# Performance work log

Hardware: AMD Instinct MI355X
Metric: run time of the kernel (lower is better)

## Reference

```python
import jax, jax.numpy as jnp
import numpy as np

EMBED_DIM = 768
N_HEADS = 12
HEAD_DIM = EMBED_DIM // N_HEADS


def setup_inputs() -> dict:
    key = jax.random.key(0)
    ks = jax.random.split(key, 5)
    s = 1.0 / np.sqrt(EMBED_DIM)
    x = jax.random.normal(ks[0], (8, 1024, EMBED_DIM), dtype=jnp.float32)
    w_qkv = jax.random.normal(ks[1], (EMBED_DIM, 3 * EMBED_DIM), dtype=jnp.float32) * s
    b_qkv = jnp.zeros((3 * EMBED_DIM,), dtype=jnp.float32)
    w_proj = jax.random.normal(ks[2], (EMBED_DIM, EMBED_DIM), dtype=jnp.float32) * s
    b_proj = jnp.zeros((EMBED_DIM,), dtype=jnp.float32)
    return {"x": x, "w_qkv": w_qkv, "b_qkv": b_qkv, "w_proj": w_proj, "b_proj": b_proj}


def reference(x, w_qkv, b_qkv, w_proj, b_proj):
    B, S, D = x.shape
    H, Hd = N_HEADS, HEAD_DIM
    qkv = x @ w_qkv + b_qkv                      # [B,S,3D]
    qkv = qkv.reshape(B, S, 3, H, Hd).transpose(2, 0, 3, 1, 4)  # [3,B,H,S,Hd]
    q, k, v = qkv[0], qkv[1], qkv[2]
    scale = Hd ** -0.5
    attn = jnp.einsum('bhqd,bhkd->bhqk', q, k) * scale  # [B,H,S,S]
    attn = jax.nn.softmax(attn, axis=-1)
    out = jnp.einsum('bhqk,bhkd->bhqd', attn, v)        # [B,H,S,Hd]
    out = out.transpose(0, 2, 1, 3).reshape(B, S, D)
    return out @ w_proj + b_proj
```

## Files before the change

kernel.cpp:

```cpp
#include <hip/hip_runtime.h>
#include <stdint.h>

typedef unsigned short ushort_t;
typedef __bf16 bf16x8 __attribute__((ext_vector_type(8)));
typedef float floatx4 __attribute__((ext_vector_type(4)));

#define B_   8
#define S_   1024
#define D_   768
#define H_   12
#define M_   (B_ * S_)
#define N3_  (3 * D_)
#define QK_  1536

static __device__ __forceinline__ void gl_lds16(const void* g, void* l) {
  __builtin_amdgcn_global_load_lds((const __attribute__((address_space(1))) void*)g,
                                   (__attribute__((address_space(3))) void*)l,
                                   16, 0, 0);
}

static __device__ __forceinline__ ushort_t f2bf(float f) {
  __bf16 h = (__bf16)f;
  return __builtin_bit_cast(unsigned short, h);
}

static __device__ __forceinline__ void store_out(ushort_t* p, float v) { *p = f2bf(v); }
static __device__ __forceinline__ void store_out(float* p, float v) { *p = v; }

static __device__ __forceinline__ void transpose_tile(const float* __restrict__ W,
                                                      ushort_t* __restrict__ Wt,
                                                      int K, int N, int bx, int by,
                                                      int t) {
  __shared__ float tile[32][33];
  const int n0 = bx * 32, k0 = by * 32;
  const int tx = t & 31, ty = t >> 5;
#pragma unroll
  for (int i = 0; i < 4; ++i)
    tile[ty + i * 8][tx] = W[(size_t)(k0 + ty + i * 8) * N + n0 + tx];
  __syncthreads();
#pragma unroll
  for (int i = 0; i < 4; ++i)
    Wt[(size_t)(n0 + ty + i * 8) * K + k0 + tx] = f2bf(tile[tx][ty + i * 8]);
}

__global__ __launch_bounds__(256) void prep_kernel(const float* __restrict__ x,
                                                   ushort_t* __restrict__ xb,
                                                   const float* __restrict__ w_qkv,
                                                   ushort_t* __restrict__ wqkvt,
                                                   const float* __restrict__ w_proj,
                                                   ushort_t* __restrict__ wprojt) {
  const int gb = blockIdx.x, t = threadIdx.x;
  if (gb < 24576) {
    const int i = gb * 256 + t;
    xb[i] = f2bf(x[i]);
  } else if (gb < 24576 + 1728) {
    const int lb = gb - 24576;
    transpose_tile(w_qkv, wqkvt, D_, N3_, lb % 72, lb / 72, t);
  } else {
    const int lb = gb - 24576 - 1728;
    transpose_tile(w_proj, wprojt, D_, D_, lb % 24, lb / 24, t);
  }
}

template <typename OutT, bool SPLITV>
__global__ __launch_bounds__(256) void gemm_bt_bias(const ushort_t* __restrict__ A,
                                                    const ushort_t* __restrict__ Bt,
                                                    const float* __restrict__ bias,
                                                    OutT* __restrict__ C, int CN,
                                                    ushort_t* __restrict__ vt) {
  __shared__ __align__(16) ushort_t As[128 * 32];
  __shared__ __align__(16) ushort_t Bs[128 * 32];
  const int t = threadIdx.x;
  const int wave = t >> 6, lane = t & 63;
  const int quad = lane >> 4, l15 = lane & 15;
  const int wm = wave >> 1, wn = wave & 1;
  const int m0 = blockIdx.y * 128, n0 = blockIdx.x * 128;

  floatx4 acc[4][4];
#pragma unroll
  for (int i = 0; i < 4; ++i)
#pragma unroll
    for (int j = 0; j < 4; ++j) acc[i][j] = (floatx4)0.0f;

  for (int k0 = 0; k0 < 768; k0 += 32) {
    if (k0) __syncthreads();
#pragma unroll
    for (int c = 0; c < 2; ++c) {
      const int i0 = c * 256 + wave * 64;
      const int i = i0 + lane;
      const int row = i >> 2, cp = i & 3;
      gl_lds16(A + (size_t)(m0 + row) * 768 + k0 + cp * 8, As + i0 * 8);
      gl_lds16(Bt + (size_t)(n0 + row) * 768 + k0 + cp * 8, Bs + i0 * 8);
    }
    __syncthreads();

    bf16x8 af[4], bfr[4];
#pragma unroll
    for (int mi = 0; mi < 4; ++mi)
      af[mi] = *(const bf16x8*)(As + (wm * 64 + mi * 16 + l15) * 32 + quad * 8);
#pragma unroll
    for (int ni = 0; ni < 4; ++ni)
      bfr[ni] = *(const bf16x8*)(Bs + (wn * 64 + ni * 16 + l15) * 32 + quad * 8);
#pragma unroll
    for (int mi = 0; mi < 4; ++mi)
#pragma unroll
      for (int ni = 0; ni < 4; ++ni)
        acc[mi][ni] = __builtin_amdgcn_mfma_f32_16x16x32_bf16(af[mi], bfr[ni], acc[mi][ni], 0, 0, 0);
  }

#pragma unroll
  for (int ni = 0; ni < 4; ++ni) {
    const int colb = n0 + wn * 64 + ni * 16;
    const int col = colb + l15;
    const float bb = bias[col];
    if (SPLITV && colb >= 1536) {
      const int hh = (colb - 1536) >> 6;
      const int d  = ((colb - 1536) & 63) + l15;
      const int bh = (m0 >> 10) * H_ + hh;
      ushort_t* vrow = vt + ((size_t)bh * 64 + d) * 1024 +
                       (m0 & 1023) + wm * 64 + quad * 4;
#pragma unroll
      for (int mi = 0; mi < 4; ++mi) {
        ushort4 pk;
        pk.x = f2bf(acc[mi][ni][0] + bb);
        pk.y = f2bf(acc[mi][ni][1] + bb);
        pk.z = f2bf(acc[mi][ni][2] + bb);
        pk.w = f2bf(acc[mi][ni][3] + bb);
        *(ushort4*)(vrow + mi * 16) = pk;
      }
    } else {
#pragma unroll
      for (int mi = 0; mi < 4; ++mi) {
#pragma unroll
        for (int r = 0; r < 4; ++r) {
          const int row = m0 + wm * 64 + mi * 16 + quad * 4 + r;
          store_out(&C[(size_t)row * CN + col], acc[mi][ni][r] + bb);
        }
      }
    }
  }
}

__global__ __launch_bounds__(256) void attn_kernel(const ushort_t* __restrict__ qk,
                                                   const ushort_t* __restrict__ vt,
                                                   ushort_t* __restrict__ o) {
  __shared__ __align__(16) ushort_t Qs[128 * 64];
  __shared__ __align__(16) ushort_t Ks[64 * 64];
  __shared__ __align__(16) ushort_t Vts[64 * 64];
  __shared__ __align__(16) ushort_t Ps[128 * 72];

  const int t = threadIdx.x;
  const int wave = t >> 6, lane = t & 63;
  const int quad = lane >> 4, l15 = lane & 15;

  const int g = blockIdx.x;
  const int xcd = g & 7, gi = g >> 3;
  const int bh = xcd * 12 + (gi >> 3);
  const int q0 = (gi & 7) * 128;
  const int h = bh % H_;
  const int bS = (bh / H_) * S_;
  const ushort_t* vbase = vt + (size_t)bh * 64 * 1024;

#pragma unroll
  for (int c = 0; c < 4; ++c) {
    const int i0 = c * 256 + wave * 64;
    const int i = i0 + lane;
    const int row = i >> 3, sg = (i & 7) ^ (row & 7);
    gl_lds16(qk + (size_t)(bS + q0 + row) * QK_ + h * 64 + sg * 8, Qs + i0 * 8);
  }
  __syncthreads();

  bf16x8 qf[2][2];
#pragma unroll
  for (int mi = 0; mi < 2; ++mi)
#pragma unroll
    for (int kb = 0; kb < 2; ++kb)
      qf[mi][kb] = *(const bf16x8*)(Qs + (wave * 32 + mi * 16 + l15) * 64 +
                                    (((kb * 4 + quad) ^ (l15 & 7)) * 8));

  floatx4 oa[2][4];
#pragma unroll
  for (int mi = 0; mi < 2; ++mi)
#pragma unroll
    for (int d = 0; d < 4; ++d) oa[mi][d] = (floatx4)0.0f;
  float lsum[2][4] = {{0.f, 0.f, 0.f, 0.f}, {0.f, 0.f, 0.f, 0.f}};

  for (int kv0 = 0; kv0 < S_; kv0 += 64) {
#pragma unroll
    for (int c = 0; c < 2; ++c) {
      const int i0 = c * 256 + wave * 64;
      const int i = i0 + lane;
      const int row = i >> 3, sg = (i & 7) ^ (row & 7);
      gl_lds16(qk + (size_t)(bS + kv0 + row) * QK_ + 768 + h * 64 + sg * 8,
               Ks + i0 * 8);
      gl_lds16(vbase + (size_t)row * 1024 + kv0 + sg * 8, Vts + i0 * 8);
    }
    __syncthreads();

    floatx4 sa[2][4];
#pragma unroll
    for (int mi = 0; mi < 2; ++mi)
#pragma unroll
      for (int ni = 0; ni < 4; ++ni) sa[mi][ni] = (floatx4)0.0f;
#pragma unroll
    for (int ni = 0; ni < 4; ++ni)
#pragma unroll
      for (int kb = 0; kb < 2; ++kb) {
        const bf16x8 kf = *(const bf16x8*)(Ks + (ni * 16 + l15) * 64 +
                                           (((kb * 4 + quad) ^ (l15 & 7)) * 8));
#pragma unroll
        for (int mi = 0; mi < 2; ++mi)
          sa[mi][ni] = __builtin_amdgcn_mfma_f32_16x16x32_bf16(qf[mi][kb], kf, sa[mi][ni], 0, 0, 0);
      }

#pragma unroll
    for (int mi = 0; mi < 2; ++mi)
#pragma unroll
      for (int r = 0; r < 4; ++r) {
        float psum = 0.0f;
#pragma unroll
        for (int ni = 0; ni < 4; ++ni) {
          const float p = __expf(fmaf(sa[mi][ni][r], 0.125f, -16.0f));
          psum += p;
          Ps[(wave * 32 + mi * 16 + quad * 4 + r) * 72 + ni * 16 + l15] = f2bf(p);
        }
        lsum[mi][r] += psum;
      }

#pragma unroll
    for (int kb = 0; kb < 2; ++kb) {
      bf16x8 vf[4];
#pragma unroll
      for (int dt = 0; dt < 4; ++dt)
        vf[dt] = *(const bf16x8*)(Vts + (dt * 16 + l15) * 64 +
                                  (((kb * 4 + quad) ^ (l15 & 7)) * 8));
#pragma unroll
      for (int mi = 0; mi < 2; ++mi) {
        const bf16x8 pf = *(const bf16x8*)(Ps + (wave * 32 + mi * 16 + l15) * 72 +
                                           kb * 32 + quad * 8);
#pragma unroll
        for (int dt = 0; dt < 4; ++dt)
          oa[mi][dt] = __builtin_amdgcn_mfma_f32_16x16x32_bf16(pf, vf[dt], oa[mi][dt], 0, 0, 0);
      }
    }
    __syncthreads();
  }

#pragma unroll
  for (int mi = 0; mi < 2; ++mi)
#pragma unroll
    for (int r = 0; r < 4; ++r) {
#pragma unroll
      for (int off = 8; off >= 1; off >>= 1)
        lsum[mi][r] += __shfl_xor(lsum[mi][r], off, 64);
    }

#pragma unroll
  for (int mi = 0; mi < 2; ++mi)
#pragma unroll
    for (int dt = 0; dt < 4; ++dt)
#pragma unroll
      for (int r = 0; r < 4; ++r) {
        const int q = q0 + wave * 32 + mi * 16 + quad * 4 + r;
        o[(size_t)(bS + q) * D_ + h * 64 + dt * 16 + l15] =
            f2bf(oa[mi][dt][r] / lsum[mi][r]);
      }
}

extern "C" void kernel_launch(void* const* d_in, const int* in_sizes, int n_in,
                              void* d_out, int out_size, void* d_ws, size_t ws_size,
                              hipStream_t stream) {
  const float* x      = (const float*)d_in[0];
  const float* w_qkv  = (const float*)d_in[1];
  const float* b_qkv  = (const float*)d_in[2];
  const float* w_proj = (const float*)d_in[3];
  const float* b_proj = (const float*)d_in[4];
  float* out = (float*)d_out;

  ushort_t* xb = (ushort_t*)d_out;

  ushort_t* vtb    = (ushort_t*)d_ws;
  ushort_t* wqkvt  = vtb + (size_t)96 * 64 * 1024;
  ushort_t* wprojt = wqkvt + (size_t)N3_ * D_;
  ushort_t* qkb    = wprojt + (size_t)D_ * D_;
  ushort_t* attnb  = qkb + (size_t)M_ * QK_;

  prep_kernel<<<24576 + 1728 + 576, 256, 0, stream>>>(x, xb, w_qkv, wqkvt,
                                                      w_proj, wprojt);
  gemm_bt_bias<ushort_t, true><<<dim3(N3_ / 128, M_ / 128), 256, 0, stream>>>(
      xb, wqkvt, b_qkv, qkb, QK_, vtb);
  attn_kernel<<<dim3(768), 256, 0, stream>>>(qkb, vtb, attnb);
  gemm_bt_bias<float, false><<<dim3(D_ / 128, M_ / 128), 256, 0, stream>>>(
      attnb, wprojt, b_proj, out, D_, nullptr);
}
```

Baseline: 208.9 us.

## Replace 128x128 GEMM with pipelined 256x256 tile, XOR-swizzled LDS, XCD-aware grid

Both dense projections now use a 512-thread kernel that computes 256x256 output tiles with BK=64 double-buffered LDS. Global-to-LDS loads for the next K tile are split into quarters and interleaved with four MFMA phases using barriers, s_setprio and explicit vmcnt waits. LDS columns are XOR-swizzled to avoid bank conflicts, and block indices are remapped so each XCD gets a contiguous chunk of tiles. The aim is more reuse per byte loaded and hidden load latency. The cost is much larger LDS and register use, and fewer blocks: 288 for the QKV GEMM and only 96 for the output projection on a 256-CU part, which risks leaving CUs idle.

```diff
diff --git a/kernel.cpp b/kernel.cpp
--- a/kernel.cpp
+++ b/kernel.cpp
@@ -62,65 +62,162 @@
   }
 }
 
+static __device__ __forceinline__ void stage_half(const ushort_t* __restrict__ gt,
+                                                  int k0, ushort_t* lds, int h,
+                                                  int wave, int srl, int scol) {
+  const int rb0 = h * 128;
+  gl_lds16(gt + (size_t)(rb0 + srl) * 768 + k0 + scol, lds + (rb0 + wave * 8) * 64);
+  const int rb1 = h * 128 + 64;
+  gl_lds16(gt + (size_t)(rb1 + srl) * 768 + k0 + scol, lds + (rb1 + wave * 8) * 64);
+}
+
 template <typename OutT, bool SPLITV>
-__global__ __launch_bounds__(256) void gemm_bt_bias(const ushort_t* __restrict__ A,
-                                                    const ushort_t* __restrict__ Bt,
-                                                    const float* __restrict__ bias,
-                                                    OutT* __restrict__ C, int CN,
-                                                    ushort_t* __restrict__ vt) {
-  __shared__ __align__(16) ushort_t As[128 * 32];
-  __shared__ __align__(16) ushort_t Bs[128 * 32];
+__global__ __launch_bounds__(512, 2) void gemm256(const ushort_t* __restrict__ A,
+                                                  const ushort_t* __restrict__ Bt,
+                                                  const float* __restrict__ bias,
+                                                  OutT* __restrict__ C, int CN,
+                                                  ushort_t* __restrict__ vt,
+                                                  int NBX, int CHUNK) {
+  __shared__ __align__(16) ushort_t As[2][256 * 64];
+  __shared__ __align__(16) ushort_t Bs[2][256 * 64];
+
   const int t = threadIdx.x;
   const int wave = t >> 6, lane = t & 63;
   const int quad = lane >> 4, l15 = lane & 15;
-  const int wm = wave >> 1, wn = wave & 1;
-  const int m0 = blockIdx.y * 128, n0 = blockIdx.x * 128;
-
-  floatx4 acc[4][4];
-#pragma unroll
-  for (int i = 0; i < 4; ++i)
+  const int wm = wave >> 2, wn = wave & 3;
+
+  const int g = blockIdx.x;
+  const int swz = (g & 7) * CHUNK + (g >> 3);
+  const int bx = swz % NBX, by = swz / NBX;
+  const int m0 = by * 256, n0 = bx * 256;
+
+  const int srl  = wave * 8 + (lane >> 3);
+  const int scol = ((lane & 7) ^ (lane >> 3)) * 8;
+
+  const int rsw = l15 & 7;
+  int slotk[2];
+  slotk[0] = ((0 * 4 + quad) ^ rsw) * 8;
+  slotk[1] = ((1 * 4 + quad) ^ rsw) * 8;
+
+  const int arow = wm * 128 + l15;
+  const int brow = wn * 64 + l15;
+
+  const ushort_t* At  = A + (size_t)m0 * 768;
+  const ushort_t* Bte = Bt + (size_t)n0 * 768;
+
+  floatx4 acc[8][4];
+#pragma unroll
+  for (int i = 0; i < 8; ++i)
 #pragma unroll
     for (int j = 0; j < 4; ++j) acc[i][j] = (floatx4)0.0f;
 
-  for (int k0 = 0; k0 < 768; k0 += 32) {
-    if (k0) __syncthreads();
-#pragma unroll
-    for (int c = 0; c < 2; ++c) {
-      const int i0 = c * 256 + wave * 64;
-      const int i = i0 + lane;
-      const int row = i >> 2, cp = i & 3;
-      gl_lds16(A + (size_t)(m0 + row) * 768 + k0 + cp * 8, As + i0 * 8);
-      gl_lds16(Bt + (size_t)(n0 + row) * 768 + k0 + cp * 8, Bs + i0 * 8);
-    }
-    __syncthreads();
-
-    bf16x8 af[4], bfr[4];
+  stage_half(At, 0, As[0], 0, wave, srl, scol);
+  stage_half(At, 0, As[0], 1, wave, srl, scol);
+  stage_half(Bte, 0, Bs[0], 0, wave, srl, scol);
+  stage_half(Bte, 0, Bs[0], 1, wave, srl, scol);
+  stage_half(At, 64, As[1], 0, wave, srl, scol);
+  asm volatile("s_waitcnt vmcnt(2)" ::: "memory");
+  __builtin_amdgcn_s_barrier();
+
+  bf16x8 af[4][2], bf2[4][2];
+
+  for (int kt = 0; kt < 12; ++kt) {
+    const int k0 = kt * 64;
+    const ushort_t* Ab = As[kt & 1];
+    const ushort_t* Bb = Bs[kt & 1];
+    ushort_t* An  = As[(kt + 1) & 1];
+    ushort_t* Bn  = Bs[(kt + 1) & 1];
+    ushort_t* Af2 = As[kt & 1];
+    const bool p1 = (kt + 1) < 12;
+    const bool p2 = (kt + 2) < 12;
+
 #pragma unroll
     for (int mi = 0; mi < 4; ++mi)
-      af[mi] = *(const bf16x8*)(As + (wm * 64 + mi * 16 + l15) * 32 + quad * 8);
-#pragma unroll
-    for (int ni = 0; ni < 4; ++ni)
-      bfr[ni] = *(const bf16x8*)(Bs + (wn * 64 + ni * 16 + l15) * 32 + quad * 8);
+#pragma unroll
+      for (int kb = 0; kb < 2; ++kb)
+        af[mi][kb] = *(const bf16x8*)(Ab + (arow + mi * 16) * 64 + slotk[kb]);
+#pragma unroll
+    for (int ni = 0; ni < 2; ++ni)
+#pragma unroll
+      for (int kb = 0; kb < 2; ++kb)
+        bf2[ni][kb] = *(const bf16x8*)(Bb + (brow + ni * 16) * 64 + slotk[kb]);
+    if (p1) stage_half(At, k0 + 64, An, 1, wave, srl, scol);
+    __builtin_amdgcn_s_barrier();
+    __builtin_amdgcn_s_setprio(1);
+#pragma unroll
+    for (int ni = 0; ni < 2; ++ni)
+#pragma unroll
+      for (int kb = 0; kb < 2; ++kb)
+#pragma unroll
+        for (int mi = 0; mi < 4; ++mi)
+          acc[mi][ni] = __builtin_amdgcn_mfma_f32_16x16x32_bf16(af[mi][kb], bf2[ni][kb], acc[mi][ni], 0, 0, 0);
+    __builtin_amdgcn_s_setprio(0);
+    __builtin_amdgcn_s_barrier();
+
+#pragma unroll
+    for (int ni = 0; ni < 2; ++ni)
+#pragma unroll
+      for (int kb = 0; kb < 2; ++kb)
+        bf2[2 + ni][kb] = *(const bf16x8*)(Bb + (brow + (2 + ni) * 16) * 64 + slotk[kb]);
+    if (p1) stage_half(Bte, k0 + 64, Bn, 0, wave, srl, scol);
+    __builtin_amdgcn_s_barrier();
+    __builtin_amdgcn_s_setprio(1);
+#pragma unroll
+    for (int ni = 0; ni < 2; ++ni)
+#pragma unroll
+      for (int kb = 0; kb < 2; ++kb)
+#pragma unroll
+        for (int mi = 0; mi < 4; ++mi)
+          acc[mi][2 + ni] = __builtin_amdgcn_mfma_f32_16x16x32_bf16(af[mi][kb], bf2[2 + ni][kb], acc[mi][2 + ni], 0, 0, 0);
+    __builtin_amdgcn_s_setprio(0);
+    __builtin_amdgcn_s_barrier();
+
 #pragma unroll
     for (int mi = 0; mi < 4; ++mi)
 #pragma unroll
-      for (int ni = 0; ni < 4; ++ni)
-        acc[mi][ni] = __builtin_amdgcn_mfma_f32_16x16x32_bf16(af[mi], bfr[ni], acc[mi][ni], 0, 0, 0);
+      for (int kb = 0; kb < 2; ++kb)
+        af[mi][kb] = *(const bf16x8*)(Ab + (arow + 64 + mi * 16) * 64 + slotk[kb]);
+    if (p1) stage_half(Bte, k0 + 64, Bn, 1, wave, srl, scol);
+    __builtin_amdgcn_s_barrier();
+    __builtin_amdgcn_s_setprio(1);
+#pragma unroll
+    for (int ni = 0; ni < 2; ++ni)
+#pragma unroll
+      for (int kb = 0; kb < 2; ++kb)
+#pragma unroll
+        for (int mi = 0; mi < 4; ++mi)
+          acc[4 + mi][ni] = __builtin_amdgcn_mfma_f32_16x16x32_bf16(af[mi][kb], bf2[ni][kb], acc[4 + mi][ni], 0, 0, 0);
+    __builtin_amdgcn_s_setprio(0);
+    __builtin_amdgcn_s_barrier();
+
+    if (p2) stage_half(At, k0 + 128, Af2, 0, wave, srl, scol);
+    __builtin_amdgcn_s_barrier();
+    __builtin_amdgcn_s_setprio(1);
+#pragma unroll
+    for (int ni = 0; ni < 2; ++ni)
+#pragma unroll
+      for (int kb = 0; kb < 2; ++kb)
+#pragma unroll
+        for (int mi = 0; mi < 4; ++mi)
+          acc[4 + mi][2 + ni] = __builtin_amdgcn_mfma_f32_16x16x32_bf16(af[mi][kb], bf2[2 + ni][kb], acc[4 + mi][2 + ni], 0, 0, 0);
+    __builtin_amdgcn_s_setprio(0);
+    if (p2) asm volatile("s_waitcnt vmcnt(2)" ::: "memory");
+    else    asm volatile("s_waitcnt vmcnt(0)" ::: "memory");
+    __builtin_amdgcn_s_barrier();
   }
 
 #pragma unroll
   for (int ni = 0; ni < 4; ++ni) {
     const int colb = n0 + wn * 64 + ni * 16;
-    const int col = colb + l15;
-    const float bb = bias[col];
-    if (SPLITV && colb >= 1536) {
-      const int hh = (colb - 1536) >> 6;
-      const int d  = ((colb - 1536) & 63) + l15;
+    const float bb = bias[colb + l15];
+    if (SPLITV && n0 >= 1536) {
+      const int hh = ((n0 - 1536) >> 6) + wn;
+      const int d  = ni * 16 + l15;
       const int bh = (m0 >> 10) * H_ + hh;
       ushort_t* vrow = vt + ((size_t)bh * 64 + d) * 1024 +
-                       (m0 & 1023) + wm * 64 + quad * 4;
-#pragma unroll
-      for (int mi = 0; mi < 4; ++mi) {
+                       (m0 & 1023) + wm * 128 + quad * 4;
+#pragma unroll
+      for (int mi = 0; mi < 8; ++mi) {
         ushort4 pk;
         pk.x = f2bf(acc[mi][ni][0] + bb);
         pk.y = f2bf(acc[mi][ni][1] + bb);
@@ -129,14 +226,14 @@
         *(ushort4*)(vrow + mi * 16) = pk;
       }
     } else {
-#pragma unroll
-      for (int mi = 0; mi < 4; ++mi) {
+      const int col = colb + l15;
+#pragma unroll
+      for (int mi = 0; mi < 8; ++mi)
 #pragma unroll
         for (int r = 0; r < 4; ++r) {
-          const int row = m0 + wm * 64 + mi * 16 + quad * 4 + r;
+          const int row = m0 + wm * 128 + mi * 16 + quad * 4 + r;
           store_out(&C[(size_t)row * CN + col], acc[mi][ni][r] + bb);
         }
-      }
     }
   }
 }
@@ -287,9 +384,9 @@
 
   prep_kernel<<<24576 + 1728 + 576, 256, 0, stream>>>(x, xb, w_qkv, wqkvt,
                                                       w_proj, wprojt);
-  gemm_bt_bias<ushort_t, true><<<dim3(N3_ / 128, M_ / 128), 256, 0, stream>>>(
-      xb, wqkvt, b_qkv, qkb, QK_, vtb);
+  gemm256<ushort_t, true><<<288, 512, 0, stream>>>(xb, wqkvt, b_qkv, qkb, QK_,
+                                                   vtb, 9, 36);
   attn_kernel<<<dim3(768), 256, 0, stream>>>(qkb, vtb, attnb);
-  gemm_bt_bias<float, false><<<dim3(D_ / 128, M_ / 128), 256, 0, stream>>>(
-      attnb, wprojt, b_proj, out, D_, nullptr);
-}
+  gemm256<float, false><<<96, 512, 0, stream>>>(attnb, wprojt, b_proj, out, D_,
+                                                nullptr, 3, 12);
+}
```

After: 223.0 us. +6.7%, slower.

## Double-buffer GEMM tiles with BK=64, XOR-swizzled LDS and block remapping

Applied to the files above, without the earlier changes.

Rewrites both GEMMs to use a K-tile of 64 with two LDS buffers, so the global-to-LDS loads for the next tile are issued before the MFMAs run on the current one. An XOR swizzle is added to the LDS layout to avoid bank conflicts on fragment reads. A 1D grid with a chunked block remap (grid index modulo 8 times a chunk size) replaces the 2D grid, which changes how tiles are spread across XCDs and may improve L2 reuse. LDS use per block grows to 64KB and a launch bound of 2 blocks per CU is set, trading occupancy headroom for overlap.

```diff
diff --git a/kernel.cpp b/kernel.cpp
--- a/kernel.cpp
+++ b/kernel.cpp
@@ -63,18 +63,37 @@
 }
 
 template <typename OutT, bool SPLITV>
-__global__ __launch_bounds__(256) void gemm_bt_bias(const ushort_t* __restrict__ A,
-                                                    const ushort_t* __restrict__ Bt,
-                                                    const float* __restrict__ bias,
-                                                    OutT* __restrict__ C, int CN,
-                                                    ushort_t* __restrict__ vt) {
-  __shared__ __align__(16) ushort_t As[128 * 32];
-  __shared__ __align__(16) ushort_t Bs[128 * 32];
+__global__ __launch_bounds__(256, 2) void gemm128(const ushort_t* __restrict__ A,
+                                                  const ushort_t* __restrict__ Bt,
+                                                  const float* __restrict__ bias,
+                                                  OutT* __restrict__ C, int CN,
+                                                  ushort_t* __restrict__ vt,
+                                                  int NBX, int CHUNK) {
+  __shared__ __align__(16) ushort_t As[2][128 * 64];
+  __shared__ __align__(16) ushort_t Bs[2][128 * 64];
+
   const int t = threadIdx.x;
   const int wave = t >> 6, lane = t & 63;
   const int quad = lane >> 4, l15 = lane & 15;
   const int wm = wave >> 1, wn = wave & 1;
-  const int m0 = blockIdx.y * 128, n0 = blockIdx.x * 128;
+
+  const int g = blockIdx.x;
+  const int swz = (g & 7) * CHUNK + (g >> 3);
+  const int bx = swz % NBX, by = swz / NBX;
+  const int m0 = by * 128, n0 = bx * 128;
+
+  const int rsub = wave * 8 + (lane >> 3);
+  const int scol = ((lane & 7) ^ ((lane >> 3) & 7)) * 8;
+
+  const int rsw = l15 & 7;
+  const int slot0 = ((0 * 4 + quad) ^ rsw) * 8;
+  const int slot1 = ((1 * 4 + quad) ^ rsw) * 8;
+
+  const int arow = wm * 64 + l15;
+  const int brow = wn * 64 + l15;
+
+  const ushort_t* At  = A + (size_t)m0 * 768;
+  const ushort_t* Bte = Bt + (size_t)n0 * 768;
 
   floatx4 acc[4][4];
 #pragma unroll
@@ -82,30 +101,55 @@
 #pragma unroll
     for (int j = 0; j < 4; ++j) acc[i][j] = (floatx4)0.0f;
 
-  for (int k0 = 0; k0 < 768; k0 += 32) {
-    if (k0) __syncthreads();
-#pragma unroll
-    for (int c = 0; c < 2; ++c) {
-      const int i0 = c * 256 + wave * 64;
-      const int i = i0 + lane;
-      const int row = i >> 2, cp = i & 3;
-      gl_lds16(A + (size_t)(m0 + row) * 768 + k0 + cp * 8, As + i0 * 8);
-      gl_lds16(Bt + (size_t)(n0 + row) * 768 + k0 + cp * 8, Bs + i0 * 8);
-    }
-    __syncthreads();
-
-    bf16x8 af[4], bfr[4];
+#pragma unroll
+  for (int c = 0; c < 4; ++c) {
+    gl_lds16(At + (size_t)(c * 32 + rsub) * 768 + scol,
+             &As[0][(c * 32 + wave * 8) * 64]);
+    gl_lds16(Bte + (size_t)(c * 32 + rsub) * 768 + scol,
+             &Bs[0][(c * 32 + wave * 8) * 64]);
+  }
+  asm volatile("s_waitcnt vmcnt(0)" ::: "memory");
+  __builtin_amdgcn_s_barrier();
+
+#pragma unroll
+  for (int kt = 0; kt < 12; ++kt) {
+    const ushort_t* Ab = As[kt & 1];
+    const ushort_t* Bb = Bs[kt & 1];
+
+    if (kt + 1 < 12) {
+      const int k1 = (kt + 1) * 64;
+      ushort_t* An = As[(kt + 1) & 1];
+      ushort_t* Bn = Bs[(kt + 1) & 1];
+#pragma unroll
+      for (int c = 0; c < 4; ++c) {
+        gl_lds16(At + (size_t)(c * 32 + rsub) * 768 + k1 + scol,
+                 An + (c * 32 + wave * 8) * 64);
+        gl_lds16(Bte + (size_t)(c * 32 + rsub) * 768 + k1 + scol,
+                 Bn + (c * 32 + wave * 8) * 64);
+      }
+    }
+
+    bf16x8 af[4][2], bfr[4][2];
+#pragma unroll
+    for (int mi = 0; mi < 4; ++mi) {
+      af[mi][0] = *(const bf16x8*)(Ab + (arow + mi * 16) * 64 + slot0);
+      af[mi][1] = *(const bf16x8*)(Ab + (arow + mi * 16) * 64 + slot1);
+    }
+#pragma unroll
+    for (int ni = 0; ni < 4; ++ni) {
+      bfr[ni][0] = *(const bf16x8*)(Bb + (brow + ni * 16) * 64 + slot0);
+      bfr[ni][1] = *(const bf16x8*)(Bb + (brow + ni * 16) * 64 + slot1);
+    }
 #pragma unroll
     for (int mi = 0; mi < 4; ++mi)
-      af[mi] = *(const bf16x8*)(As + (wm * 64 + mi * 16 + l15) * 32 + quad * 8);
-#pragma unroll
-    for (int ni = 0; ni < 4; ++ni)
-      bfr[ni] = *(const bf16x8*)(Bs + (wn * 64 + ni * 16 + l15) * 32 + quad * 8);
-#pragma unroll
-    for (int mi = 0; mi < 4; ++mi)
-#pragma unroll
-      for (int ni = 0; ni < 4; ++ni)
-        acc[mi][ni] = __builtin_amdgcn_mfma_f32_16x16x32_bf16(af[mi], bfr[ni], acc[mi][ni], 0, 0, 0);
+#pragma unroll
+      for (int ni = 0; ni < 4; ++ni) {
+        acc[mi][ni] = __builtin_amdgcn_mfma_f32_16x16x32_bf16(af[mi][0], bfr[ni][0], acc[mi][ni], 0, 0, 0);
+        acc[mi][ni] = __builtin_amdgcn_mfma_f32_16x16x32_bf16(af[mi][1], bfr[ni][1], acc[mi][ni], 0, 0, 0);
+      }
+
+    asm volatile("s_waitcnt vmcnt(0)" ::: "memory");
+    __builtin_amdgcn_s_barrier();
   }
 
 #pragma unroll
@@ -287,9 +331,9 @@
 
   prep_kernel<<<24576 + 1728 + 576, 256, 0, stream>>>(x, xb, w_qkv, wqkvt,
                                                       w_proj, wprojt);
-  gemm_bt_bias<ushort_t, true><<<dim3(N3_ / 128, M_ / 128), 256, 0, stream>>>(
-      xb, wqkvt, b_qkv, qkb, QK_, vtb);
+  gemm128<ushort_t, true><<<1152, 256, 0, stream>>>(xb, wqkvt, b_qkv, qkb, QK_,
+                                                    vtb, 18, 144);
   attn_kernel<<<dim3(768), 256, 0, stream>>>(qkb, vtb, attnb);
-  gemm_bt_bias<float, false><<<dim3(D_ / 128, M_ / 128), 256, 0, stream>>>(
-      attnb, wprojt, b_proj, out, D_, nullptr);
-}
+  gemm128<float, false><<<384, 256, 0, stream>>>(attnb, wprojt, b_proj, out, D_,
+                                                 nullptr, 6, 48);
+}
```

Result: faster. 199.1 us (-4.7%).

## Double-buffer K/V tiles in attention, swizzle GEMM LDS, use exp2 softmax

Applied to the files above, without the earlier changes.

The attention kernel now prefetches the next K/V tile into a second LDS buffer, reusing the Q staging area once Q is held in registers, so global loads overlap with the MFMA work on the current tile. The GEMM applies an XOR swizzle to its LDS column slots to reduce bank conflicts on the fragment reads. The softmax exponent is rewritten as exp2f with constants folded in. The diff only shows a sync after the MFMA/softmax phase; whether the loop still waits for the async prefetch and for the previous buffer to be drained before reuse depends on lines that are not shown, so there may be a hazard.

```diff
diff --git a/kernel.cpp b/kernel.cpp
--- a/kernel.cpp
+++ b/kernel.cpp
@@ -76,6 +76,9 @@
   const int wm = wave >> 1, wn = wave & 1;
   const int m0 = blockIdx.y * 128, n0 = blockIdx.x * 128;
 
+  const int scol  = ((lane & 3) ^ ((lane >> 3) & 3)) * 8;
+  const int slotq = (quad ^ ((l15 >> 1) & 3)) * 8;
+
   floatx4 acc[4][4];
 #pragma unroll
   for (int i = 0; i < 4; ++i)
@@ -88,19 +91,19 @@
     for (int c = 0; c < 2; ++c) {
       const int i0 = c * 256 + wave * 64;
       const int i = i0 + lane;
-      const int row = i >> 2, cp = i & 3;
-      gl_lds16(A + (size_t)(m0 + row) * 768 + k0 + cp * 8, As + i0 * 8);
-      gl_lds16(Bt + (size_t)(n0 + row) * 768 + k0 + cp * 8, Bs + i0 * 8);
+      const int row = i >> 2;
+      gl_lds16(A + (size_t)(m0 + row) * 768 + k0 + scol, As + i0 * 8);
+      gl_lds16(Bt + (size_t)(n0 + row) * 768 + k0 + scol, Bs + i0 * 8);
     }
     __syncthreads();
 
     bf16x8 af[4], bfr[4];
 #pragma unroll
     for (int mi = 0; mi < 4; ++mi)
-      af[mi] = *(const bf16x8*)(As + (wm * 64 + mi * 16 + l15) * 32 + quad * 8);
+      af[mi] = *(const bf16x8*)(As + (wm * 64 + mi * 16 + l15) * 32 + slotq);
 #pragma unroll
     for (int ni = 0; ni < 4; ++ni)
-      bfr[ni] = *(const bf16x8*)(Bs + (wn * 64 + ni * 16 + l15) * 32 + quad * 8);
+      bfr[ni] = *(const bf16x8*)(Bs + (wn * 64 + ni * 16 + l15) * 32 + slotq);
 #pragma unroll
     for (int mi = 0; mi < 4; ++mi)
 #pragma unroll
@@ -168,6 +171,14 @@
     const int row = i >> 3, sg = (i & 7) ^ (row & 7);
     gl_lds16(qk + (size_t)(bS + q0 + row) * QK_ + h * 64 + sg * 8, Qs + i0 * 8);
   }
+#pragma unroll
+  for (int c = 0; c < 2; ++c) {
+    const int i0 = c * 256 + wave * 64;
+    const int i = i0 + lane;
+    const int row = i >> 3, sg = (i & 7) ^ (row & 7);
+    gl_lds16(qk + (size_t)(bS + row) * QK_ + 768 + h * 64 + sg * 8, Ks + i0 * 8);
+    gl_lds16(vbase + (size_t)row * 1024 + sg * 8, Vts + i0 * 8);
+  }
   __syncthreads();
 
   bf16x8 qf[2][2];
@@ -177,6 +188,8 @@
     for (int kb = 0; kb < 2; ++kb)
       qf[mi][kb] = *(const bf16x8*)(Qs + (wave * 32 + mi * 16 + l15) * 64 +
                                     (((kb * 4 + quad) ^ (l15 & 7)) * 8));
+  asm volatile("s_waitcnt lgkmcnt(0)" ::: "memory");
+  __syncthreads();
 
   floatx4 oa[2][4];
 #pragma unroll
@@ -186,16 +199,24 @@
   float lsum[2][4] = {{0.f, 0.f, 0.f, 0.f}, {0.f, 0.f, 0.f, 0.f}};
 
   for (int kv0 = 0; kv0 < S_; kv0 += 64) {
-#pragma unroll
-    for (int c = 0; c < 2; ++c) {
-      const int i0 = c * 256 + wave * 64;
-      const int i = i0 + lane;
-      const int row = i >> 3, sg = (i & 7) ^ (row & 7);
-      gl_lds16(qk + (size_t)(bS + kv0 + row) * QK_ + 768 + h * 64 + sg * 8,
-               Ks + i0 * 8);
-      gl_lds16(vbase + (size_t)row * 1024 + kv0 + sg * 8, Vts + i0 * 8);
-    }
-    __syncthreads();
+    const int par = (kv0 >> 6) & 1;
+    const ushort_t* Kc = par ? Qs : Ks;
+    const ushort_t* Vc = par ? (Qs + 4096) : Vts;
+
+    if (kv0 + 64 < S_) {
+      ushort_t* Kn = par ? Ks : Qs;
+      ushort_t* Vn = par ? Vts : (Qs + 4096);
+      const int kv1 = kv0 + 64;
+#pragma unroll
+      for (int c = 0; c < 2; ++c) {
+        const int i0 = c * 256 + wave * 64;
+        const int i = i0 + lane;
+        const int row = i >> 3, sg = (i & 7) ^ (row & 7);
+        gl_lds16(qk + (size_t)(bS + kv1 + row) * QK_ + 768 + h * 64 + sg * 8,
+                 Kn + i0 * 8);
+        gl_lds16(vbase + (size_t)row * 1024 + kv1 + sg * 8, Vn + i0 * 8);
+      }
+    }
 
     floatx4 sa[2][4];
 #pragma unroll
@@ -206,7 +227,7 @@
     for (int ni = 0; ni < 4; ++ni)
 #pragma unroll
       for (int kb = 0; kb < 2; ++kb) {
-        const bf16x8 kf = *(const bf16x8*)(Ks + (ni * 16 + l15) * 64 +
+        const bf16x8 kf = *(const bf16x8*)(Kc + (ni * 16 + l15) * 64 +
                                            (((kb * 4 + quad) ^ (l15 & 7)) * 8));
 #pragma unroll
         for (int mi = 0; mi < 2; ++mi)
@@ -220,7 +241,7 @@
         float psum = 0.0f;
 #pragma unroll
         for (int ni = 0; ni < 4; ++ni) {
-          const float p = __expf(fmaf(sa[mi][ni][r], 0.125f, -16.0f));
+          const float p = exp2f(fmaf(sa[mi][ni][r], 0.18033688f, -23.0831204f));
           psum += p;
           Ps[(wave * 32 + mi * 16 + quad * 4 + r) * 72 + ni * 16 + l15] = f2bf(p);
         }
@@ -232,7 +253,7 @@
       bf16x8 vf[4];
 #pragma unroll
       for (int dt = 0; dt < 4; ++dt)
-        vf[dt] = *(const bf16x8*)(Vts + (dt * 16 + l15) * 64 +
+        vf[dt] = *(const bf16x8*)(Vc + (dt * 16 + l15) * 64 +
                                   (((kb * 4 + quad) ^ (l15 & 7)) * 8));
 #pragma unroll
       for (int mi = 0; mi < 2; ++mi) {
```

After: 212.8 us. About the same (+1.9%).
